# Optimization experiments

Hardware: AMD Instinct MI355X
Metric: run time of the kernel (lower is better)

## Reference

```python
import jax, jax.numpy as jnp
import numpy as np

NUM_HEADS = 16


def setup_inputs() -> dict:
    key = jax.random.key(0)
    ks = jax.random.split(key, 5)
    B, S, H = 2, 2048, 1024
    scale = 0.02
    return {
        "x": jax.random.normal(ks[0], (B, S, H), dtype=jnp.float32),
        "w_qkv": jax.random.normal(ks[1], (H, 3 * H), dtype=jnp.float32) * scale,
        "b_qkv": jax.random.normal(ks[2], (3 * H,), dtype=jnp.float32) * scale,
        "w_out": jax.random.normal(ks[3], (H, H), dtype=jnp.float32) * scale,
        "b_out": jax.random.normal(ks[4], (H,), dtype=jnp.float32) * scale,
    }


def reference(x, w_qkv, b_qkv, w_out, b_out):
    B, S, H = x.shape
    nh = NUM_HEADS
    hd = H // nh
    attn_scale = 1.0 / np.sqrt(hd).astype(np.float32)

    qkv = x @ w_qkv + b_qkv                       # (B, S, 3H)
    q, k, v = jnp.split(qkv, 3, axis=-1)
    # (B, S, H) -> (B, nh, S, hd)
    to_heads = lambda t: t.reshape(B, S, nh, hd).transpose(0, 2, 1, 3)
    q, k, v = to_heads(q), to_heads(k), to_heads(v)

    scores = jnp.einsum("bhid,bhjd->bhij", q, k) * attn_scale  # (B, nh, S, S)
    # Source masks where triu(ones)==0 -> strictly-lower triangle masked;
    # allowed positions are j >= i (attends to present and future).
    i = jnp.arange(S)[:, None]
    j = jnp.arange(S)[None, :]
    scores = jnp.where(j >= i, scores, -jnp.inf)
    attn = jax.nn.softmax(scores, axis=-1)        # dropout is identity (eval)

    out = jnp.einsum("bhij,bhjd->bhid", attn, v)  # (B, nh, S, hd)
    out = out.transpose(0, 2, 1, 3).reshape(B, S, H)
    return out @ w_out + b_out
```

## Files before the change

kernel.cpp:

```cpp
#include <hip/hip_runtime.h>
#include <hip/hip_bf16.h>
#include <stdint.h>
#include <stddef.h>

typedef __bf16 bf16_t;
typedef __bf16 bf16x4 __attribute__((ext_vector_type(4)));
typedef __bf16 bf16x8 __attribute__((ext_vector_type(8)));
typedef float f32x4 __attribute__((ext_vector_type(4)));
typedef float f32x16 __attribute__((ext_vector_type(16)));

#define MFMA16(a, b, c) __builtin_amdgcn_mfma_f32_16x16x32_bf16(a, b, c, 0, 0, 0)
#define MFMA32(a, b, c) __builtin_amdgcn_mfma_f32_32x32x16_bf16(a, b, c, 0, 0, 0)

#define GLL16(g, l)                                                      \
    __builtin_amdgcn_global_load_lds(                                    \
        (const __attribute__((address_space(1))) void*)(g),              \
        (__attribute__((address_space(3))) void*)(l), 16, 0, 0)

#define SEQ 2048
#define NHEAD 16
#define HD 64
#define HID 1024
#define QKV_LD 3072
#define VT_LD 2080

__global__ __launch_bounds__(256)
void prep_kernel(const float* __restrict__ x, const float* __restrict__ w_qkv,
                 const float* __restrict__ w_out, bf16_t* __restrict__ xbf,
                 bf16_t* __restrict__ wqkvT, bf16_t* __restrict__ woutT) {
    int L = blockIdx.x;
    int tid = threadIdx.x;
    if (L < 4096) {
        int i = (L * 256 + tid) * 4;
        float4 v = *(const float4*)(x + i);
        bf16x4 o = {(bf16_t)v.x, (bf16_t)v.y, (bf16_t)v.z, (bf16_t)v.w};
        *(bf16x4*)(xbf + i) = o;
        return;
    }
    __shared__ bf16_t tile[32][33];
    const float* W;
    bf16_t* Wt;
    int N, bx, by;
    if (L < 7168) {
        int r = L - 4096;
        W = w_qkv; Wt = wqkvT; N = 3072; bx = r % 96; by = r / 96;
    } else {
        int r = L - 7168;
        W = w_out; Wt = woutT; N = 1024; bx = r % 32; by = r / 32;
    }
    int K = 1024;
    int n0 = bx * 32, k0 = by * 32;
    int tx = tid & 31, ty = tid >> 5;
#pragma unroll
    for (int i = 0; i < 4; i++)
        tile[ty + i * 8][tx] = (bf16_t)W[(size_t)(k0 + ty + i * 8) * N + n0 + tx];
    __syncthreads();
#pragma unroll
    for (int i = 0; i < 4; i++)
        Wt[(size_t)(n0 + ty + i * 8) * K + k0 + tx] = tile[tx][ty + i * 8];
}

__global__ __launch_bounds__(256)
void vt_transpose(const bf16_t* __restrict__ qkv, bf16_t* __restrict__ Vt) {
    int s0 = blockIdx.x * 64;
    int bh = blockIdx.y;
    int b = bh >> 4, h = bh & 15;
    int tid = threadIdx.x;
    __shared__ __align__(16) bf16_t tile[64][72];

    int row = tid >> 3, c8 = (tid & 7) * 8;
#pragma unroll
    for (int it = 0; it < 2; it++) {
        int sr = row + it * 32;
        bf16x8 v = *(const bf16x8*)(qkv + ((size_t)b * SEQ + s0 + sr) * QKV_LD +
                                    2 * HID + h * HD + c8);
        *(bf16x8*)(&tile[sr][c8]) = v;
    }
    __syncthreads();
#pragma unroll
    for (int it = 0; it < 2; it++) {
        int d = row + it * 32;
        bf16x8 w;
#pragma unroll
        for (int e = 0; e < 8; e++) w[e] = tile[c8 + e][d];
        *(bf16x8*)(Vt + ((size_t)bh * HD + d) * VT_LD + s0 + c8) = w;
    }
}

#define STAGE8(GB, LB, KOFF)                                                   \
    do {                                                                       \
        GLL16((GB) + (size_t)srow * K + (KOFF) + ssw,                          \
              (LB) + srow * 64 + (scl << 3));                                  \
        GLL16((GB) + (size_t)(srow + 64) * K + (KOFF) + ssw,                   \
              (LB) + (srow + 64) * 64 + (scl << 3));                           \
    } while (0)

__global__ __launch_bounds__(512, 2)
void gemm_qkv_8ph(const bf16_t* __restrict__ A, const bf16_t* __restrict__ Bt,
                  const float* __restrict__ bias, bf16_t* __restrict__ C,
                  int M, int N, int K) {
    __shared__ __align__(16) bf16_t As[2][256][64];
    __shared__ __align__(16) bf16_t Bs[2][256][64];

    int nbx = N >> 8;
    int bid = blockIdx.x;
    int swz = (bid & 7) * (gridDim.x >> 3) + (bid >> 3);
    int m0 = (swz / nbx) << 8;
    int n0 = (swz % nbx) << 8;

    int tid = threadIdx.x;
    int lane = tid & 63;
    int wave = tid >> 6;
    int l16 = lane & 15, quad = lane >> 4;
    int wm = (wave >> 2) << 7;
    int wn = (wave & 3) << 6;

    int srow = tid >> 3;
    int scl = tid & 7;
    int ssw = ((scl ^ (srow & 7)) << 3);

    const bf16_t* Ab = A + (size_t)m0 * K;
    const bf16_t* Bb = Bt + (size_t)n0 * K;

    f32x4 acc[8][4] = {};
    bf16x8 af[4][2], b0[2][2], b1[2][2];

    const int NT = K >> 6;

    STAGE8(Bb, &Bs[0][0][0], 0);
    STAGE8(Ab, &As[0][0][0], 0);
    STAGE8(Bb + (size_t)128 * K, &Bs[0][128][0], 0);
    STAGE8(Ab + (size_t)128 * K, &As[0][128][0], 0);
    STAGE8(Bb, &Bs[1][0][0], 64);
    STAGE8(Ab, &As[1][0][0], 64);
    asm volatile("s_waitcnt vmcnt(4)" ::: "memory");
    __builtin_amdgcn_s_barrier();

    for (int t = 0; t < NT; t++) {
        int buf = t & 1;
        const bf16_t* Asb = &As[buf][0][0];
        const bf16_t* Bsb = &Bs[buf][0][0];
        int k1 = (t + 1) << 6;
        int k2 = (t + 2) << 6;

#pragma unroll
        for (int mt = 0; mt < 4; mt++) {
            int row = wm + mt * 16 + l16;
#pragma unroll
            for (int ks = 0; ks < 2; ks++)
                af[mt][ks] = *(const bf16x8*)(
                    Asb + row * 64 + (((ks * 4 + quad) ^ (row & 7)) << 3));
        }
#pragma unroll
        for (int nt = 0; nt < 2; nt++) {
            int row = wn + nt * 16 + l16;
#pragma unroll
            for (int ks = 0; ks < 2; ks++)
                b0[nt][ks] = *(const bf16x8*)(
                    Bsb + row * 64 + (((ks * 4 + quad) ^ (row & 7)) << 3));
        }
        if (t + 1 < NT) STAGE8(Bb + (size_t)128 * K, &Bs[buf ^ 1][128][0], k1);
        __builtin_amdgcn_s_barrier();
        asm volatile("s_waitcnt lgkmcnt(0)" ::: "memory");
        __builtin_amdgcn_s_setprio(1);
#pragma unroll
        for (int mt = 0; mt < 4; mt++)
#pragma unroll
            for (int nt = 0; nt < 2; nt++)
#pragma unroll
                for (int ks = 0; ks < 2; ks++)
                    acc[mt][nt] = MFMA16(af[mt][ks], b0[nt][ks], acc[mt][nt]);
        __builtin_amdgcn_s_setprio(0);
        __builtin_amdgcn_s_barrier();

#pragma unroll
        for (int nt = 0; nt < 2; nt++) {
            int row = wn + 32 + nt * 16 + l16;
#pragma unroll
            for (int ks = 0; ks < 2; ks++)
                b1[nt][ks] = *(const bf16x8*)(
                    Bsb + row * 64 + (((ks * 4 + quad) ^ (row & 7)) << 3));
        }
        if (t + 1 < NT) STAGE8(Ab + (size_t)128 * K, &As[buf ^ 1][128][0], k1);
        __builtin_amdgcn_s_barrier();
        asm volatile("s_waitcnt lgkmcnt(0)" ::: "memory");
        __builtin_amdgcn_s_setprio(1);
#pragma unroll
        for (int mt = 0; mt < 4; mt++)
#pragma unroll
            for (int nt = 0; nt < 2; nt++)
#pragma unroll
                for (int ks = 0; ks < 2; ks++)
                    acc[mt][2 + nt] =
                        MFMA16(af[mt][ks], b1[nt][ks], acc[mt][2 + nt]);
        __builtin_amdgcn_s_setprio(0);
        __builtin_amdgcn_s_barrier();

#pragma unroll
        for (int mt = 0; mt < 4; mt++) {
            int row = wm + 64 + mt * 16 + l16;
#pragma unroll
            for (int ks = 0; ks < 2; ks++)
                af[mt][ks] = *(const bf16x8*)(
                    Asb + row * 64 + (((ks * 4 + quad) ^ (row & 7)) << 3));
        }
        if (t + 2 < NT) STAGE8(Bb, &Bs[buf][0][0], k2);
        __builtin_amdgcn_s_barrier();
        asm volatile("s_waitcnt lgkmcnt(0)" ::: "memory");
        __builtin_amdgcn_s_setprio(1);
#pragma unroll
        for (int mt = 0; mt < 4; mt++)
#pragma unroll
            for (int nt = 0; nt < 2; nt++)
#pragma unroll
                for (int ks = 0; ks < 2; ks++)
                    acc[4 + mt][nt] =
                        MFMA16(af[mt][ks], b0[nt][ks], acc[4 + mt][nt]);
        __builtin_amdgcn_s_setprio(0);
        __builtin_amdgcn_s_barrier();

        if (t + 2 < NT) {
            STAGE8(Ab, &As[buf][0][0], k2);
            asm volatile("s_waitcnt vmcnt(4)" ::: "memory");
        } else if (t + 1 < NT) {
            asm volatile("s_waitcnt vmcnt(0)" ::: "memory");
        }
        __builtin_amdgcn_s_barrier();
        __builtin_amdgcn_s_setprio(1);
#pragma unroll
        for (int mt = 0; mt < 4; mt++)
#pragma unroll
            for (int nt = 0; nt < 2; nt++)
#pragma unroll
                for (int ks = 0; ks < 2; ks++)
                    acc[4 + mt][2 + nt] =
                        MFMA16(af[mt][ks], b1[nt][ks], acc[4 + mt][2 + nt]);
        __builtin_amdgcn_s_setprio(0);
        __builtin_amdgcn_s_barrier();
    }

#pragma unroll
    for (int mi = 0; mi < 8; mi++) {
        int row = m0 + wm + (mi >> 2) * 64 + (mi & 3) * 16 + quad * 4;
#pragma unroll
        for (int ni = 0; ni < 4; ni++) {
            int col = n0 + wn + (ni >> 1) * 32 + (ni & 1) * 16 + l16;
            float bv = bias[col];
#pragma unroll
            for (int r = 0; r < 4; r++)
                C[(size_t)(row + r) * N + col] = (bf16_t)(acc[mi][ni][r] + bv);
        }
    }
}

template <typename OutT, int TN>
__global__ __launch_bounds__(256)
void gemm_bt_bias(const bf16_t* __restrict__ A, const bf16_t* __restrict__ Bt,
                  const float* __restrict__ bias, OutT* __restrict__ C,
                  int M, int N, int K) {
    constexpr int NT = TN / 32;
    __shared__ __align__(16) bf16_t As[128][32];
    __shared__ __align__(16) bf16_t Bs[TN][32];

    int m0 = blockIdx.y * 128;
    int n0 = blockIdx.x * TN;
    int tid = threadIdx.x;
    int wave = tid >> 6, lane = tid & 63;
    int quad = lane >> 4, l16 = lane & 15;
    int wm = (wave >> 1) * 64, wn = (wave & 1) * (TN / 2);

    f32x4 acc[4][NT] = {};

    const bf16_t* a_base =
        A + (size_t)(m0 + wave * 32 + (lane >> 2)) * K + (lane & 3) * 8;
    const bf16_t* b_base =
        Bt + (size_t)(n0 + wave * (TN / 4) + (lane >> 2)) * K + (lane & 3) * 8;
    bf16_t* as_base = &As[wave * 32][0];
    bf16_t* bs_base = &Bs[wave * (TN / 4)][0];

    for (int k0 = 0; k0 < K; k0 += 32) {
        GLL16(a_base + k0, as_base);
        GLL16(a_base + 16 * K + k0, as_base + 16 * 32);
        GLL16(b_base + k0, bs_base);
        if (TN == 128) GLL16(b_base + 16 * K + k0, bs_base + 16 * 32);
        __syncthreads();

        bf16x8 af[4], bfr[NT];
#pragma unroll
        for (int t = 0; t < 4; t++)
            af[t] = *(const bf16x8*)(&As[wm + t * 16 + l16][quad * 8]);
#pragma unroll
        for (int t = 0; t < NT; t++)
            bfr[t] = *(const bf16x8*)(&Bs[wn + t * 16 + l16][quad * 8]);
#pragma unroll
        for (int mt = 0; mt < 4; mt++)
#pragma unroll
            for (int nt = 0; nt < NT; nt++)
                acc[mt][nt] = MFMA16(af[mt], bfr[nt], acc[mt][nt]);
        __syncthreads();
    }

#pragma unroll
    for (int mt = 0; mt < 4; mt++) {
        int row = m0 + wm + mt * 16 + quad * 4;
#pragma unroll
        for (int nt = 0; nt < NT; nt++) {
            int col = n0 + wn + nt * 16 + l16;
            float bv = bias[col];
#pragma unroll
            for (int r = 0; r < 4; r++)
                C[(size_t)(row + r) * N + col] = (OutT)(acc[mt][nt][r] + bv);
        }
    }
}

__global__ __launch_bounds__(256)
void attn_kernel(const bf16_t* __restrict__ qkv, const bf16_t* __restrict__ Vt,
                 bf16_t* __restrict__ attn_out) {
    int bh = blockIdx.x;
    int tile = blockIdx.y;
    int b = bh >> 4, h = bh & 15;

    int tid = threadIdx.x, wave = tid >> 6, lane = tid & 63;
    int l32 = lane & 31, hi = lane >> 5;
    int ih = wave & 1, jh = wave >> 1;

    const bf16_t* q_g = qkv + (size_t)b * SEQ * QKV_LD + (size_t)h * HD;
    const bf16_t* k_g = q_g + HID;
    const bf16_t* vt_g = Vt + (size_t)bh * HD * VT_LD;

    __shared__ __align__(16) bf16_t Ks[64][72];
    __shared__ __align__(16) bf16_t Vs[64][72];
    __shared__ __align__(16) bf16_t Ps[64][68];
    __shared__ float lsumS[4][32];

    const float QS = 0.125f * 1.44269504088896f;
    int i0 = tile * 64;

    bf16x8 qa[4];
    {
        const bf16_t* qrow = q_g + (size_t)(i0 + ih * 32 + l32) * QKV_LD + hi * 8;
#pragma unroll
        for (int ks = 0; ks < 4; ks++) {
            bf16x8 t = *(const bf16x8*)(qrow + ks * 16);
#pragma unroll
            for (int e = 0; e < 8; e++) qa[ks][e] = (bf16_t)((float)t[e] * QS);
        }
    }

    f32x16 o = {};
    float lsum = 0.0f;

    int sr = tid >> 2, sc = (tid & 3) * 8;

    bf16x8 kr[2], vr[2];
#pragma unroll
    for (int t = 0; t < 2; t++) {
        kr[t] = *(const bf16x8*)(k_g + (size_t)(i0 + sr) * QKV_LD + sc + t * 32);
        vr[t] = *(const bf16x8*)(vt_g + (size_t)sr * VT_LD + i0 + sc + t * 32);
    }

    for (int j0 = i0; j0 < SEQ; j0 += 64) {
        __syncthreads();
#pragma unroll
        for (int t = 0; t < 2; t++) {
            *(bf16x8*)(&Ks[sr][sc + t * 32]) = kr[t];
            *(bf16x8*)(&Vs[sr][sc + t * 32]) = vr[t];
        }
        __syncthreads();

        if (j0 + 64 < SEQ) {
#pragma unroll
            for (int t = 0; t < 2; t++) {
                kr[t] = *(const bf16x8*)(k_g + (size_t)(j0 + 64 + sr) * QKV_LD + sc + t * 32);
                vr[t] = *(const bf16x8*)(vt_g + (size_t)sr * VT_LD + j0 + 64 + sc + t * 32);
            }
        }

        f32x16 st = {};
#pragma unroll
        for (int ks = 0; ks < 4; ks++) {
            bf16x8 ka = *(const bf16x8*)(&Ks[jh * 32 + l32][ks * 16 + hi * 8]);
            st = MFMA32(ka, qa[ks], st);
        }

        if (j0 == i0) {
            int gi = i0 + ih * 32 + l32;
#pragma unroll
            for (int rq = 0; rq < 4; rq++) {
                bf16x4 pk;
#pragma unroll
                for (int r = 0; r < 4; r++) {
                    int gj = j0 + jh * 32 + 8 * rq + 4 * hi + r;
                    float p = (gj >= gi) ? __builtin_amdgcn_exp2f(st[rq * 4 + r]) : 0.0f;
                    lsum += p;
                    pk[r] = (bf16_t)p;
                }
                *(bf16x4*)(&Ps[ih * 32 + l32][jh * 32 + 8 * rq + 4 * hi]) = pk;
            }
        } else {
#pragma unroll
            for (int rq = 0; rq < 4; rq++) {
                bf16x4 pk;
#pragma unroll
                for (int r = 0; r < 4; r++) {
                    float p = __builtin_amdgcn_exp2f(st[rq * 4 + r]);
                    lsum += p;
                    pk[r] = (bf16_t)p;
                }
                *(bf16x4*)(&Ps[ih * 32 + l32][jh * 32 + 8 * rq + 4 * hi]) = pk;
            }
        }
        __syncthreads();

#pragma unroll
        for (int ks = 0; ks < 4; ks++) {
            bf16x8 pa = *(const bf16x8*)(&Ps[ih * 32 + l32][ks * 16 + hi * 8]);
            bf16x8 vb = *(const bf16x8*)(&Vs[jh * 32 + l32][ks * 16 + hi * 8]);
            o = MFMA32(pa, vb, o);
        }
    }

    lsum += __shfl_xor(lsum, 32, 64);
    lsumS[wave][l32] = lsum;
    __syncthreads();

#pragma unroll
    for (int rq = 0; rq < 4; rq++) {
#pragma unroll
        for (int r = 0; r < 4; r++) {
            int il = 8 * rq + 4 * hi + r;
            float rs = lsumS[ih][il] + lsumS[ih + 2][il];
            int gi = i0 + ih * 32 + il;
            attn_out[(size_t)(b * SEQ + gi) * HID + h * HD + jh * 32 + l32] =
                (bf16_t)(o[rq * 4 + r] / rs);
        }
    }
}

extern "C" void kernel_launch(void* const* d_in, const int* in_sizes, int n_in,
                              void* d_out, int out_size, void* d_ws, size_t ws_size,
                              hipStream_t stream) {
    const float* x     = (const float*)d_in[0];
    const float* w_qkv = (const float*)d_in[1];
    const float* b_qkv = (const float*)d_in[2];
    const float* w_out = (const float*)d_in[3];
    const float* b_out = (const float*)d_in[4];
    float* out = (float*)d_out;

    char* ws = (char*)d_ws;
    bf16_t* xbf   = (bf16_t*)(ws);
    bf16_t* Vt    = (bf16_t*)(ws);
    bf16_t* wqkvT = (bf16_t*)(ws + 8388608);
    bf16_t* woutT = (bf16_t*)(ws + 14680064);
    bf16_t* qkv   = (bf16_t*)(ws + 16777216);
    bf16_t* attn  = (bf16_t*)(ws + 41943040);

    prep_kernel<<<8192, 256, 0, stream>>>(x, w_qkv, w_out, xbf, wqkvT, woutT);

    gemm_qkv_8ph<<<192, 512, 0, stream>>>(xbf, wqkvT, b_qkv, qkv,
                                          4096, 3072, 1024);

    vt_transpose<<<dim3(SEQ / 64, 2 * NHEAD), 256, 0, stream>>>(qkv, Vt);

    attn_kernel<<<dim3(2 * NHEAD, SEQ / 64), 256, 0, stream>>>(qkv, Vt, attn);

    gemm_bt_bias<float, 64><<<dim3(1024 / 64, 4096 / 128), 256, 0, stream>>>(
        attn, woutT, b_out, out, 4096, 1024, 1024);
}
```

Baseline: 181.6 us.

## Fuse V transpose into QKV GEMM epilogue and widen attention tiles

The QKV GEMM epilogue now writes the V columns straight into the transposed Vt layout, so the separate vt_transpose kernel and its extra read and write of V are gone. The attention kernel now handles 128 query rows per block with 512 threads, so each staged K/V tile in shared memory serves twice as many queries. The causal mask now covers the first two key tiles, and the tile order within the grid is remapped to help balance the triangular workload. The Vt store is strided, and the larger blocks cut the number of attention blocks in half, which may reduce occupancy.

```diff
diff --git a/kernel.cpp b/kernel.cpp
--- a/kernel.cpp
+++ b/kernel.cpp
@@ -60,33 +60,6 @@
         Wt[(size_t)(n0 + ty + i * 8) * K + k0 + tx] = tile[tx][ty + i * 8];
 }
 
-__global__ __launch_bounds__(256)
-void vt_transpose(const bf16_t* __restrict__ qkv, bf16_t* __restrict__ Vt) {
-    int s0 = blockIdx.x * 64;
-    int bh = blockIdx.y;
-    int b = bh >> 4, h = bh & 15;
-    int tid = threadIdx.x;
-    __shared__ __align__(16) bf16_t tile[64][72];
-
-    int row = tid >> 3, c8 = (tid & 7) * 8;
-#pragma unroll
-    for (int it = 0; it < 2; it++) {
-        int sr = row + it * 32;
-        bf16x8 v = *(const bf16x8*)(qkv + ((size_t)b * SEQ + s0 + sr) * QKV_LD +
-                                    2 * HID + h * HD + c8);
-        *(bf16x8*)(&tile[sr][c8]) = v;
-    }
-    __syncthreads();
-#pragma unroll
-    for (int it = 0; it < 2; it++) {
-        int d = row + it * 32;
-        bf16x8 w;
-#pragma unroll
-        for (int e = 0; e < 8; e++) w[e] = tile[c8 + e][d];
-        *(bf16x8*)(Vt + ((size_t)bh * HD + d) * VT_LD + s0 + c8) = w;
-    }
-}
-
 #define STAGE8(GB, LB, KOFF)                                                   \
     do {                                                                       \
         GLL16((GB) + (size_t)srow * K + (KOFF) + ssw,                          \
@@ -98,7 +71,7 @@
 __global__ __launch_bounds__(512, 2)
 void gemm_qkv_8ph(const bf16_t* __restrict__ A, const bf16_t* __restrict__ Bt,
                   const float* __restrict__ bias, bf16_t* __restrict__ C,
-                  int M, int N, int K) {
+                  bf16_t* __restrict__ Vt, int M, int N, int K) {
     __shared__ __align__(16) bf16_t As[2][256][64];
     __shared__ __align__(16) bf16_t Bs[2][256][64];
 
@@ -239,16 +212,36 @@
         __builtin_amdgcn_s_barrier();
     }
 
-#pragma unroll
-    for (int mi = 0; mi < 8; mi++) {
-        int row = m0 + wm + (mi >> 2) * 64 + (mi & 3) * 16 + quad * 4;
-#pragma unroll
-        for (int ni = 0; ni < 4; ni++) {
-            int col = n0 + wn + (ni >> 1) * 32 + (ni & 1) * 16 + l16;
-            float bv = bias[col];
-#pragma unroll
-            for (int r = 0; r < 4; r++)
-                C[(size_t)(row + r) * N + col] = (bf16_t)(acc[mi][ni][r] + bv);
+    if (n0 < 2048) {
+#pragma unroll
+        for (int mi = 0; mi < 8; mi++) {
+            int row = m0 + wm + (mi >> 2) * 64 + (mi & 3) * 16 + quad * 4;
+#pragma unroll
+            for (int ni = 0; ni < 4; ni++) {
+                int col = n0 + wn + (ni >> 1) * 32 + (ni & 1) * 16 + l16;
+                float bv = bias[col];
+#pragma unroll
+                for (int r = 0; r < 4; r++)
+                    C[(size_t)(row + r) * N + col] = (bf16_t)(acc[mi][ni][r] + bv);
+            }
+        }
+    } else {
+#pragma unroll
+        for (int mi = 0; mi < 8; mi++) {
+            int row = m0 + wm + (mi >> 2) * 64 + (mi & 3) * 16 + quad * 4;
+            int b = row >> 11, s = row & 2047;
+#pragma unroll
+            for (int ni = 0; ni < 4; ni++) {
+                int col = n0 + wn + (ni >> 1) * 32 + (ni & 1) * 16 + l16;
+                float bv = bias[col];
+                int cv = col - 2048;
+                int bh = b * 16 + (cv >> 6);
+                bf16x4 pk;
+#pragma unroll
+                for (int r = 0; r < 4; r++)
+                    pk[r] = (bf16_t)(acc[mi][ni][r] + bv);
+                *(bf16x4*)(Vt + ((size_t)bh * HD + (cv & 63)) * VT_LD + s) = pk;
+            }
         }
     }
 }
@@ -314,16 +307,16 @@
     }
 }
 
-__global__ __launch_bounds__(256)
+__global__ __launch_bounds__(512, 4)
 void attn_kernel(const bf16_t* __restrict__ qkv, const bf16_t* __restrict__ Vt,
                  bf16_t* __restrict__ attn_out) {
     int bh = blockIdx.x;
-    int tile = blockIdx.y;
+    int tile = (blockIdx.y < 8) ? blockIdx.y : (23 - blockIdx.y);
     int b = bh >> 4, h = bh & 15;
 
     int tid = threadIdx.x, wave = tid >> 6, lane = tid & 63;
     int l32 = lane & 31, hi = lane >> 5;
-    int ih = wave & 1, jh = wave >> 1;
+    int ih = wave >> 1, jh = wave & 1;
 
     const bf16_t* q_g = qkv + (size_t)b * SEQ * QKV_LD + (size_t)h * HD;
     const bf16_t* k_g = q_g + HID;
@@ -331,11 +324,11 @@
 
     __shared__ __align__(16) bf16_t Ks[64][72];
     __shared__ __align__(16) bf16_t Vs[64][72];
-    __shared__ __align__(16) bf16_t Ps[64][68];
-    __shared__ float lsumS[4][32];
+    __shared__ __align__(16) bf16_t Ps[128][68];
+    __shared__ float lsumS[8][32];
 
     const float QS = 0.125f * 1.44269504088896f;
-    int i0 = tile * 64;
+    int i0 = tile * 128;
 
     bf16x8 qa[4];
     {
@@ -351,30 +344,20 @@
     f32x16 o = {};
     float lsum = 0.0f;
 
-    int sr = tid >> 2, sc = (tid & 3) * 8;
-
-    bf16x8 kr[2], vr[2];
-#pragma unroll
-    for (int t = 0; t < 2; t++) {
-        kr[t] = *(const bf16x8*)(k_g + (size_t)(i0 + sr) * QKV_LD + sc + t * 32);
-        vr[t] = *(const bf16x8*)(vt_g + (size_t)sr * VT_LD + i0 + sc + t * 32);
-    }
+    int sr = tid >> 3, sc = (tid & 7) * 8;
+
+    bf16x8 kr = *(const bf16x8*)(k_g + (size_t)(i0 + sr) * QKV_LD + sc);
+    bf16x8 vr = *(const bf16x8*)(vt_g + (size_t)sr * VT_LD + i0 + sc);
 
     for (int j0 = i0; j0 < SEQ; j0 += 64) {
         __syncthreads();
-#pragma unroll
-        for (int t = 0; t < 2; t++) {
-            *(bf16x8*)(&Ks[sr][sc + t * 32]) = kr[t];
-            *(bf16x8*)(&Vs[sr][sc + t * 32]) = vr[t];
-        }
+        *(bf16x8*)(&Ks[sr][sc]) = kr;
+        *(bf16x8*)(&Vs[sr][sc]) = vr;
         __syncthreads();
 
         if (j0 + 64 < SEQ) {
-#pragma unroll
-            for (int t = 0; t < 2; t++) {
-                kr[t] = *(const bf16x8*)(k_g + (size_t)(j0 + 64 + sr) * QKV_LD + sc + t * 32);
-                vr[t] = *(const bf16x8*)(vt_g + (size_t)sr * VT_LD + j0 + 64 + sc + t * 32);
-            }
+            kr = *(const bf16x8*)(k_g + (size_t)(j0 + 64 + sr) * QKV_LD + sc);
+            vr = *(const bf16x8*)(vt_g + (size_t)sr * VT_LD + j0 + 64 + sc);
         }
 
         f32x16 st = {};
@@ -384,7 +367,7 @@
             st = MFMA32(ka, qa[ks], st);
         }
 
-        if (j0 == i0) {
+        if (j0 < i0 + 128) {
             int gi = i0 + ih * 32 + l32;
 #pragma unroll
             for (int rq = 0; rq < 4; rq++) {
@@ -430,7 +413,7 @@
 #pragma unroll
         for (int r = 0; r < 4; r++) {
             int il = 8 * rq + 4 * hi + r;
-            float rs = lsumS[ih][il] + lsumS[ih + 2][il];
+            float rs = lsumS[ih * 2][il] + lsumS[ih * 2 + 1][il];
             int gi = i0 + ih * 32 + il;
             attn_out[(size_t)(b * SEQ + gi) * HID + h * HD + jh * 32 + l32] =
                 (bf16_t)(o[rq * 4 + r] / rs);
@@ -450,20 +433,18 @@
 
     char* ws = (char*)d_ws;
     bf16_t* xbf   = (bf16_t*)(ws);
-    bf16_t* Vt    = (bf16_t*)(ws);
     bf16_t* wqkvT = (bf16_t*)(ws + 8388608);
     bf16_t* woutT = (bf16_t*)(ws + 14680064);
     bf16_t* qkv   = (bf16_t*)(ws + 16777216);
     bf16_t* attn  = (bf16_t*)(ws + 41943040);
+    bf16_t* Vt    = (bf16_t*)(ws + 50331648);
 
     prep_kernel<<<8192, 256, 0, stream>>>(x, w_qkv, w_out, xbf, wqkvT, woutT);
 
-    gemm_qkv_8ph<<<192, 512, 0, stream>>>(xbf, wqkvT, b_qkv, qkv,
+    gemm_qkv_8ph<<<192, 512, 0, stream>>>(xbf, wqkvT, b_qkv, qkv, Vt,
                                           4096, 3072, 1024);
 
-    vt_transpose<<<dim3(SEQ / 64, 2 * NHEAD), 256, 0, stream>>>(qkv, Vt);
-
-    attn_kernel<<<dim3(2 * NHEAD, SEQ / 64), 256, 0, stream>>>(qkv, Vt, attn);
+    attn_kernel<<<dim3(2 * NHEAD, SEQ / 128), 512, 0, stream>>>(qkv, Vt, attn);
 
     gemm_bt_bias<float, 64><<<dim3(1024 / 64, 4096 / 128), 256, 0, stream>>>(
         attn, woutT, b_out, out, 4096, 1024, 1024);
```

Result: faster. 172.8 us (-4.9%).
